# Kernel optimization log

Hardware: AMD Instinct MI355X
Metric: run time of the kernel (lower is better)

The kernel has to match this reference:

```python
import jax, jax.numpy as jnp
import numpy as np

D_MODEL = 768
D_AU = 5
D_VIS = 20
BOT = 64
WIN = 7
SCALE = 1.0 / np.sqrt(BOT).astype(np.float32)


def layernorm(x, w, b, eps=1e-5):
    mu = jnp.mean(x, axis=-1, keepdims=True)
    var = jnp.mean(jnp.square(x - mu), axis=-1, keepdims=True)
    return (x - mu) * jax.lax.rsqrt(var + eps) * w + b


def proximity_bias_matrix(prox_bias, L_a, L_v):
    # |i * (L_v/L_a) - j|, floored to int; gather into learned table, -inf outside window
    ai = jnp.arange(L_a, dtype=jnp.float32) * (L_v / L_a)  # [L_a]
    vj = jnp.arange(L_v, dtype=jnp.float32)                # [L_v]
    dist = jnp.floor(jnp.abs(ai[:, None] - vj[None, :])).astype(jnp.int32)  # [L_a, L_v]
    within = dist <= WIN
    gathered = prox_bias[jnp.clip(dist, 0, 2 * WIN)]
    return jnp.where(within, gathered, -jnp.inf)


def setup_inputs() -> dict:
    key = jax.random.key(0)
    ks = jax.random.split(key, 32)
    B, L_t, L_v, L_a = 32, 1024, 1024, 2048
    std = 0.02
    inp = {
        'x_text': jax.random.normal(ks[0], (B, L_t, D_MODEL), jnp.float32),
        'video_features': jax.random.normal(ks[1], (B, L_v, D_VIS), jnp.float32),
        'audio_features': jax.random.normal(ks[2], (B, L_a, D_AU), jnp.float32),
        # adapter input LayerNorm (BERT init: weight=1, bias=0)
        'ln_w': jnp.ones((D_MODEL,), jnp.float32),
        'ln_b': jnp.zeros((D_MODEL,), jnp.float32),
        # down projections (torch Linear: [out, in])
        'dpa_w': std * jax.random.normal(ks[3], (BOT, D_AU), jnp.float32),
        'dpa_b': jnp.zeros((BOT,), jnp.float32),
        'dpv_w': std * jax.random.normal(ks[4], (BOT, D_VIS), jnp.float32),
        'dpv_b': jnp.zeros((BOT,), jnp.float32),
        # audio->video cross attention
        'wq_a': std * jax.random.normal(ks[5], (BOT, BOT), jnp.float32),
        'wk_v': std * jax.random.normal(ks[6], (BOT, BOT), jnp.float32),
        'wv_v': std * jax.random.normal(ks[7], (BOT, BOT), jnp.float32),
        'prox_bias': jnp.zeros((2 * WIN + 1,), jnp.float32),
        # fusion MLP + LN
        'fln_w': jnp.ones((2 * BOT,), jnp.float32),
        'fln_b': jnp.zeros((2 * BOT,), jnp.float32),
        'w1f_w': std * jax.random.normal(ks[8], (BOT, 2 * BOT), jnp.float32),
        'w1f_b': jnp.zeros((BOT,), jnp.float32),
        'w2f_w': std * jax.random.normal(ks[9], (BOT, BOT), jnp.float32),
        'w2f_b': jnp.zeros((BOT,), jnp.float32),
        # text->sync alignment attention
        'wq_t': std * jax.random.normal(ks[10], (BOT, D_MODEL), jnp.float32),
        'wk_s': std * jax.random.normal(ks[11], (BOT, BOT), jnp.float32),
        'wv_s': std * jax.random.normal(ks[12], (BOT, BOT), jnp.float32),
        # up projection + learnable scalar
        'up_w': std * jax.random.normal(ks[13], (D_MODEL, BOT), jnp.float32),
        'up_b': jnp.zeros((D_MODEL,), jnp.float32),
        'scale': jnp.ones((1,), jnp.float32),
    }
    return inp


def reference(x_text, video_features, audio_features, ln_w, ln_b, dpa_w, dpa_b,
              dpv_w, dpv_b, wq_a, wk_v, wv_v, prox_bias, fln_w, fln_b,
              w1f_w, w1f_b, w2f_w, w2f_b, wq_t, wk_s, wv_s, up_w, up_b, scale):
    L_v = video_features.shape[1]
    L_a = audio_features.shape[1]
    # adapter_layernorm_option == 'in'
    xt = layernorm(x_text, ln_w, ln_b)
    # down projections + ReLU
    H_v = jax.nn.relu(jnp.einsum('bvf,df->bvd', video_features, dpv_w) + dpv_b)
    H_a = jax.nn.relu(jnp.einsum('baf,df->bad', audio_features, dpa_w) + dpa_b)
    # audio queries attend to video keys/values with proximity bias
    Q_a = jnp.einsum('bad,ed->bae', H_a, wq_a)
    K_v = jnp.einsum('bvd,ed->bve', H_v, wk_v)
    V_v = jnp.einsum('bvd,ed->bve', H_v, wv_v)
    scores = jnp.einsum('bad,bvd->bav', Q_a, K_v) * SCALE
    scores = scores + proximity_bias_matrix(prox_bias, L_a, L_v)[None]
    A = jax.nn.softmax(scores, axis=-1)  # dropout: eval-mode identity
    H_v_tilde = jnp.einsum('bav,bvd->bad', A, V_v)
    # fusion
    H_av = jnp.concatenate([H_a, H_v_tilde], axis=-1)  # [B, L_a, 2*BOT]
    H_av_n = layernorm(H_av, fln_w, fln_b)
    H_fused = jax.nn.relu(jnp.einsum('bac,dc->bad', H_av_n, w1f_w) + w1f_b)
    H_sync = jnp.einsum('bad,ed->bae', H_fused, w2f_w) + w2f_b
    # text -> sync alignment attention
    Q_t = jnp.einsum('btm,dm->btd', xt, wq_t)
    K_s = jnp.einsum('bad,ed->bae', H_sync, wk_s)
    V_s = jnp.einsum('bad,ed->bae', H_sync, wv_s)
    align = jax.nn.softmax(jnp.einsum('btd,bad->bta', Q_t, K_s) * SCALE, axis=-1)
    H_align = jnp.einsum('bta,bad->btd', align, V_s)
    up = jnp.einsum('btd,md->btm', H_align, up_w) + up_b
    return up * scale
```

## Files before the change

kernel.cpp:

```cpp
#include <hip/hip_runtime.h>

typedef unsigned short u16;
typedef unsigned int u32;

using frag8 = __attribute__((ext_vector_type(8))) short;
using facc4 = __attribute__((ext_vector_type(4))) float;

__device__ __forceinline__ float b2f(u16 u) {
  union { u32 i; float f; } v; v.i = ((u32)u) << 16; return v.f;
}
__device__ __forceinline__ u16 f2b(float f) {
  union { float f; u32 i; } v; v.f = f;
  u32 u = v.i;
  return (u16)((u + 0x7FFFu + ((u >> 16) & 1u)) >> 16);
}
__device__ __forceinline__ float ldin(const void* p, size_t i, bool bf) {
  return bf ? b2f(((const u16*)p)[i]) : ((const float*)p)[i];
}
__device__ __forceinline__ u16 ldb(const void* p, size_t i, bool bf) {
  return bf ? ((const u16*)p)[i] : f2b(((const float*)p)[i]);
}
__device__ __forceinline__ bool dt_bf16(const void* ones) {
  return *(const u32*)ones == 0x3F803F80u;
}
__device__ __forceinline__ void gload_lds16(const void* g, void* l) {
  __builtin_amdgcn_global_load_lds(
      (__attribute__((address_space(1))) void*)(g),
      (__attribute__((address_space(3))) void*)(l), 16, 0, 0);
}

#define LT 1024
#define LV 1024
#define LA 2048
#define DM 768

#define W_QA 0
#define W_KV 4096
#define W_VV 8192
#define W_1F 12288
#define W_2F 20480
#define W_KS 24576
#define W_VS 28672
#define W_UP 32768
#define W_QT 81920
#define W_TOT 131072

__global__ __launch_bounds__(256) void k_prep(
    const void* __restrict__ wqa, const void* __restrict__ wkv, const void* __restrict__ wvv,
    const void* __restrict__ w1f, const void* __restrict__ w2f,
    const void* __restrict__ wks, const void* __restrict__ wvs,
    const void* __restrict__ wup, const void* __restrict__ wqt, const void* __restrict__ lnw,
    u16* __restrict__ W)
{
  bool bf = dt_bf16(lnw);
  int idx = blockIdx.x * 256 + threadIdx.x;
  if (idx >= W_TOT) return;
  u16 v;
  if      (idx < W_KV) v = ldb(wqa, idx - W_QA, bf);
  else if (idx < W_VV) v = ldb(wkv, idx - W_KV, bf);
  else if (idx < W_1F) v = ldb(wvv, idx - W_VV, bf);
  else if (idx < W_2F) v = ldb(w1f, idx - W_1F, bf);
  else if (idx < W_KS) v = ldb(w2f, idx - W_2F, bf);
  else if (idx < W_VS) v = ldb(wks, idx - W_KS, bf);
  else if (idx < W_UP) v = ldb(wvs, idx - W_VS, bf);
  else if (idx < W_QT) v = ldb(wup, idx - W_UP, bf);
  else {
    int r = idx - W_QT;
    int k = r - (r / DM) * DM;
    v = f2b(ldin(wqt, r, bf) * ldin(lnw, k, bf));
  }
  W[idx] = v;
}

__global__ __launch_bounds__(256) void k_const(
    const u16* __restrict__ W, const void* __restrict__ wqt, const void* __restrict__ lnb,
    const void* __restrict__ dtp, float* __restrict__ CC)
{
  bool bf = dt_bf16(dtp);
  int j = blockIdx.x * 8 + (threadIdx.x >> 5);
  int lane32 = threadIdx.x & 31;
  float s = 0.f;
  if (j < 64) {
    for (int k = lane32; k < DM; k += 32) s += b2f(W[W_QT + (size_t)j * DM + k]);
  } else {
    int e = j - 64;
    for (int k = lane32; k < DM; k += 32)
      s += ldin(lnb, k, bf) * ldin(wqt, (size_t)e * DM + k, bf);
  }
#pragma unroll
  for (int m = 1; m < 32; m <<= 1) s += __shfl_xor(s, m);
  if (lane32 == 0) CC[j] = s;
}

__global__ __launch_bounds__(256) void k_video(
    const void* __restrict__ vid, const void* __restrict__ dpv_w, const void* __restrict__ dpv_b,
    const u16* __restrict__ W, const void* __restrict__ dtp,
    u16* __restrict__ KvG, u16* __restrict__ VvTG)
{
  bool bf = dt_bf16(dtp);
  __shared__ float vidT[20][72];
  __shared__ float dpvT[20][72];
  __shared__ float dpvB[64];
  __shared__ u16 hvL[64][72];
  __shared__ u16 ksS[64][72];
  __shared__ u16 vsS[64][72];
  int tid = threadIdx.x;
  int b = blockIdx.x >> 4, v0 = (blockIdx.x & 15) << 6;
  for (int c = tid; c < 1280; c += 256) {
    int row = c / 20, d = c - row * 20;
    vidT[d][row] = ldin(vid, (size_t)(b * LV + v0) * 20 + c, bf);
    dpvT[d][row] = ldin(dpv_w, c, bf);
  }
  if (tid < 64) dpvB[tid] = ldin(dpv_b, tid, bf);
  __syncthreads();
  int w = tid >> 6, ln = tid & 63;
  int quad = ln >> 4, l16 = ln & 15;
  for (int rr = 0; rr < 16; ++rr) {
    int row = w * 16 + rr;
    float h = dpvB[ln];
#pragma unroll
    for (int d = 0; d < 20; ++d) h += vidT[d][row] * dpvT[d][ln];
    hvL[row][ln] = f2b(fmaxf(h, 0.f));
  }
  facc4 ka[4] = {}, va[4] = {};
#pragma unroll
  for (int kk = 0; kk < 2; ++kk) {
    frag8 af = *(const frag8*)&hvL[w * 16 + l16][kk * 32 + quad * 8];
#pragma unroll
    for (int nt = 0; nt < 4; ++nt) {
      frag8 bk = *(const frag8*)(W + W_KV + (size_t)(nt * 16 + l16) * 64 + kk * 32 + quad * 8);
      frag8 bv = *(const frag8*)(W + W_VV + (size_t)(nt * 16 + l16) * 64 + kk * 32 + quad * 8);
      ka[nt] = __builtin_amdgcn_mfma_f32_16x16x32_bf16(af, bk, ka[nt], 0, 0, 0);
      va[nt] = __builtin_amdgcn_mfma_f32_16x16x32_bf16(af, bv, va[nt], 0, 0, 0);
    }
  }
#pragma unroll
  for (int nt = 0; nt < 4; ++nt)
#pragma unroll
    for (int r = 0; r < 4; ++r) {
      int row = w * 16 + quad * 4 + r;
      ksS[row][nt * 16 + l16] = f2b(ka[nt][r]);
      vsS[row][nt * 16 + l16] = f2b(va[nt][r]);
    }
  __syncthreads();
  for (int c = tid; c < 2048; c += 256) {
    int row = c >> 5, sg = c & 31;
    u32 v = (u32)ksS[row][sg * 2] | ((u32)ksS[row][sg * 2 + 1] << 16);
    *(u32*)(KvG + (size_t)(b * LV + v0 + row) * 64 + sg * 2) = v;
  }
  for (int c = tid; c < 2048; c += 256) {
    int e = c >> 5, sg = c & 31;
    u32 v = (u32)vsS[sg * 2][e] | ((u32)vsS[sg * 2 + 1][e] << 16);
    *(u32*)(VvTG + (size_t)(b * 64 + e) * LV + v0 + sg * 2) = v;
  }
}

__global__ __launch_bounds__(256, 2) void k_lnqt(
    const void* __restrict__ x, const u16* __restrict__ W, const float* __restrict__ CC,
    const void* __restrict__ dtp, u16* __restrict__ Qt)
{
  bool bf = dt_bf16(dtp);
  __shared__ __align__(16) char pool[65536];
  int tid = threadIdx.x;
  int w = tid >> 6, ln = tid & 63;
  int quad = ln >> 4, l16 = ln & 15;
  int R0 = blockIdx.x * 64;
  facc4 acc[4] = {};
  float s = 0.f, ss = 0.f;

  if (!bf) {
    int rqe = ln >> 4;
    const char* xb = (const char*)x + (size_t)R0 * 3072;
    const char* pe = xb + (size_t)(w * 16 + rqe) * 3072 + (((ln & 15) ^ rqe) << 4);
    const char* po = xb + (size_t)(w * 16 + 4 + rqe) * 3072 + (((ln & 15) ^ (4 + rqe)) << 4);
    const char* wgA = (const char*)(W + W_QT) +
        (size_t)(w * 16 + (ln >> 3)) * 1536 + (((ln & 7) ^ (ln >> 3)) << 4);
    const char* wgB = wgA + 8 * 1536;

#define STAGE_X(BUF, T) do { \
    size_t o_ = (size_t)(T) * 256; \
    char* lb_ = pool + (BUF) * 16384 + w * 4096; \
    gload_lds16(pe + o_,         lb_); \
    gload_lds16(po + o_,         lb_ + 1024); \
    gload_lds16(pe + 24576 + o_, lb_ + 2048); \
    gload_lds16(po + 24576 + o_, lb_ + 3072); \
  } while (0)

#define STAGE_W(BUF, T) do { \
    size_t o_ = (size_t)(T) * 128; \
    char* wb_ = pool + 49152 + (BUF) * 8192 + w * 2048; \
    gload_lds16(wgA + o_, wb_); \
    gload_lds16(wgB + o_, wb_ + 1024); \
  } while (0)

    int rbase = (w * 16 + l16) * 256;
    int r8 = l16 & 7;
    int c0a = rbase + (((quad * 2) ^ r8) << 4);
    int c0b = rbase + (((quad * 2 + 1) ^ r8) << 4);
    int c1a = rbase + (((8 + quad * 2) ^ r8) << 4);
    int c1b = rbase + (((9 + quad * 2) ^ r8) << 4);
    int wo0 = l16 * 128 + ((quad ^ r8) << 4);
    int wo1 = l16 * 128 + (((4 + quad) ^ r8) << 4);

#define COMPUTE(XB, WB) do { \
    const char* xt_ = pool + (XB) * 16384; \
    const char* wt_ = pool + 49152 + (WB) * 8192; \
    _Pragma("unroll") \
    for (int ks = 0; ks < 2; ++ks) { \
      float4 v0 = *(const float4*)(xt_ + (ks ? c1a : c0a)); \
      float4 v1 = *(const float4*)(xt_ + (ks ? c1b : c0b)); \
      s += v0.x + v0.y + v0.z + v0.w + v1.x + v1.y + v1.z + v1.w; \
      ss += v0.x * v0.x + v0.y * v0.y + v0.z * v0.z + v0.w * v0.w \
          + v1.x * v1.x + v1.y * v1.y + v1.z * v1.z + v1.w * v1.w; \
      union { u16 a[8]; frag8 f; } af; \
      af.a[0] = f2b(v0.x); af.a[1] = f2b(v0.y); af.a[2] = f2b(v0.z); af.a[3] = f2b(v0.w); \
      af.a[4] = f2b(v1.x); af.a[5] = f2b(v1.y); af.a[6] = f2b(v1.z); af.a[7] = f2b(v1.w); \
      int wo_ = ks ? wo1 : wo0; \
      _Pragma("unroll") \
      for (int nt = 0; nt < 4; ++nt) { \
        frag8 bfr = *(const frag8*)(wt_ + wo_ + nt * 2048); \
        acc[nt] = __builtin_amdgcn_mfma_f32_16x16x32_bf16(af.f, bfr, acc[nt], 0, 0, 0); \
      } \
    } \
  } while (0)

#define ITERA(T) do { \
    asm volatile("s_waitcnt vmcnt(4)" ::: "memory"); \
    __builtin_amdgcn_s_barrier(); \
    STAGE_W(((T) + 1) & 1, (T) + 1); \
    STAGE_X(((T) + 2) % 3, (T) + 2); \
    COMPUTE((T) % 3, (T) & 1); \
  } while (0)

    STAGE_W(0, 0);
    STAGE_X(0, 0);
    STAGE_X(1, 1);
    ITERA(0); ITERA(1); ITERA(2); ITERA(3); ITERA(4);
    ITERA(5); ITERA(6); ITERA(7); ITERA(8); ITERA(9);
    asm volatile("s_waitcnt vmcnt(4)" ::: "memory");
    __builtin_amdgcn_s_barrier();
    STAGE_W(1, 11);
    COMPUTE(1, 0);
    asm volatile("s_waitcnt vmcnt(0)" ::: "memory");
    __builtin_amdgcn_s_barrier();
    COMPUTE(2, 1);

#undef ITERA
#undef COMPUTE
#undef STAGE_W
#undef STAGE_X
  } else {
    const u16* xrowb = (const u16*)x + (size_t)(R0 + w * 16 + l16) * DM + quad * 8;
    for (int c = 0; c < 24; ++c) {
      union { u16 a[8]; frag8 f; } af;
      af.f = *(const frag8*)(xrowb + c * 32);
#pragma unroll
      for (int jj = 0; jj < 8; ++jj) { float v = b2f(af.a[jj]); s += v; ss += v * v; }
      int col = c * 32 + quad * 8;
#pragma unroll
      for (int nt = 0; nt < 4; ++nt) {
        frag8 bfr = *(const frag8*)(W + W_QT + (size_t)(nt * 16 + l16) * DM + col);
        acc[nt] = __builtin_amdgcn_mfma_f32_16x16x32_bf16(af.f, bfr, acc[nt], 0, 0, 0);
      }
    }
  }

  s += __shfl_xor(s, 16); ss += __shfl_xor(ss, 16);
  s += __shfl_xor(s, 32); ss += __shfl_xor(ss, 32);
  float mu = s * (1.f / 768.f);
  float var = ss * (1.f / 768.f) - mu * mu;
  float rs = rsqrtf(var + 1e-5f);
  float muR[4], rsR[4];
#pragma unroll
  for (int r = 0; r < 4; ++r) {
    muR[r] = __shfl(mu, quad * 4 + r);
    rsR[r] = __shfl(rs, quad * 4 + r);
  }
#pragma unroll
  for (int nt = 0; nt < 4; ++nt) {
    float c1 = CC[nt * 16 + l16], c2 = CC[64 + nt * 16 + l16];
#pragma unroll
    for (int r = 0; r < 4; ++r) {
      int lrow = w * 16 + quad * 4 + r;
      Qt[(size_t)(R0 + lrow) * 64 + nt * 16 + l16] =
          f2b((acc[nt][r] - muR[r] * c1) * rsR[r] * 0.125f + c2 * 0.125f);
    }
  }
}

__global__ __launch_bounds__(256) void k_audio(
    const void* __restrict__ audio, const void* __restrict__ dpa_w, const void* __restrict__ dpa_b,
    const void* __restrict__ prox_b,
    const void* __restrict__ fln_w, const void* __restrict__ fln_b,
    const void* __restrict__ w1f_b, const void* __restrict__ w2f_b,
    const u16* __restrict__ W, const void* __restrict__ dtp,
    const u16* __restrict__ KvG, const u16* __restrict__ VvTG,
    u16* __restrict__ KsG, u16* __restrict__ VsTG)
{
  bool bf = dt_bf16(dtp);
  __shared__ __align__(16) char pool[53056];
  u16* hL   = (u16*)pool;
  u16* kvB  = (u16*)(pool + 9216);
  u16* vvT  = (u16*)(pool + 16128);
  u16* qL   = (u16*)(pool + 25344);
  u16* hnL  = (u16*)(pool + 25344);
  u16* pfL  = (u16*)(pool + 42752);
  u16* hsS  = (u16*)(pool + 9216);
  u16* ksS  = (u16*)pool;
  u16* vsS  = (u16*)(pool + 9216);
  float* flnw = (float*)(pool + 51968);
  float* flnb = (float*)(pool + 52480);
  float* prox = (float*)(pool + 52992);

  int tid = threadIdx.x;
  int b = blockIdx.x >> 5, i0 = (blockIdx.x & 31) << 6;
  int w = tid >> 6, ln = tid & 63;
  int quad = ln >> 4, l16 = ln & 15;
  int jbase = (i0 >> 1) - 7;

  if (tid >= 64 && tid < 192) { int t = tid - 64; flnw[t] = ldin(fln_w, t, bf); flnb[t] = ldin(fln_b, t, bf); }
  if (tid >= 192 && tid < 207) prox[tid - 192] = ldin(prox_b, tid - 192, bf);
  for (int c = tid; c < 1536; c += 256) {
    int jr = c >> 5, ep = c & 31;
    int jj = jbase + jr; jj = jj < 0 ? 0 : (jj > LV - 1 ? LV - 1 : jj);
    *(u32*)&kvB[jr * 72 + ep * 2] = *(const u32*)(KvG + (size_t)(b * LV + jj) * 64 + ep * 2);
  }
  for (int c = tid; c < 3072; c += 256) {
    int e = c / 48, jw = c - e * 48;
    int jj = jbase + jw; jj = jj < 0 ? 0 : (jj > LV - 1 ? LV - 1 : jj);
    vvT[e * 72 + jw] = VvTG[(size_t)(b * 64 + e) * LV + jj];
  }
  for (int c = tid; c < 1024; c += 256) vvT[(c >> 4) * 72 + 48 + (c & 15)] = 0;
  __syncthreads();

  float haF[4][4];
  {
    frag8 au = {};
    if (quad == 0) {
      size_t base = (size_t)(b * LA + i0 + w * 16 + l16) * 5;
#pragma unroll
      for (int k = 0; k < 5; ++k) au[k] = (short)ldb(audio, base + k, bf);
    }
#pragma unroll
    for (int nt = 0; nt < 4; ++nt) {
      frag8 bd = {};
      if (quad == 0) {
#pragma unroll
        for (int k = 0; k < 5; ++k) bd[k] = (short)ldb(dpa_w, (size_t)(nt * 16 + l16) * 5 + k, bf);
      }
      facc4 z = {};
      facc4 ha = __builtin_amdgcn_mfma_f32_16x16x32_bf16(au, bd, z, 0, 0, 0);
      float dB = ldin(dpa_b, nt * 16 + l16, bf);
#pragma unroll
      for (int r = 0; r < 4; ++r) {
        u16 hb = f2b(fmaxf(ha[r] + dB, 0.f));
        hL[(w * 16 + quad * 4 + r) * 72 + nt * 16 + l16] = hb;
        haF[nt][r] = b2f(hb);
      }
    }
  }
  {
    facc4 qa[4] = {};
#pragma unroll
    for (int kk = 0; kk < 2; ++kk) {
      frag8 af = *(const frag8*)&hL[(w * 16 + l16) * 72 + kk * 32 + quad * 8];
#pragma unroll
      for (int nt = 0; nt < 4; ++nt) {
        frag8 bfr = *(const frag8*)(W + W_QA + (size_t)(nt * 16 + l16) * 64 + kk * 32 + quad * 8);
        qa[nt] = __builtin_amdgcn_mfma_f32_16x16x32_bf16(af, bfr, qa[nt], 0, 0, 0);
      }
    }
#pragma unroll
    for (int nt = 0; nt < 4; ++nt)
#pragma unroll
      for (int r = 0; r < 4; ++r)
        qL[(w * 16 + quad * 4 + r) * 72 + nt * 16 + l16] = f2b(qa[nt][r] * 0.125f);
  }
  float inv[4];
  {
    facc4 sa[3] = {};
#pragma unroll
    for (int kk = 0; kk < 2; ++kk) {
      frag8 af = *(const frag8*)&qL[(w * 16 + l16) * 72 + kk * 32 + quad * 8];
#pragma unroll
      for (int nt = 0; nt < 3; ++nt) {
        frag8 bfr = *(const frag8*)&kvB[(nt * 16 + l16) * 72 + kk * 32 + quad * 8];
        sa[nt] = __builtin_amdgcn_mfma_f32_16x16x32_bf16(af, bfr, sa[nt], 0, 0, 0);
      }
    }
    float den[4] = {0.f, 0.f, 0.f, 0.f};
#pragma unroll
    for (int nt = 0; nt < 3; ++nt)
#pragma unroll
      for (int r = 0; r < 4; ++r) {
        int row16 = quad * 4 + r;
        int i = i0 + w * 16 + row16;
        int j = jbase + nt * 16 + l16;
        float dist = fabsf((float)i * 0.5f - (float)j);
        float p = 0.f;
        if (j >= 0 && j < LV && dist < 8.f)
          p = exp2f(fminf(sa[nt][r] + prox[(int)dist], 60.f) * 1.44269504f);
        u16 pb = f2b(p);
        den[r] += b2f(pb);
        pfL[(w * 16 + row16) * 72 + nt * 16 + l16] = pb;
      }
#pragma unroll
    for (int r = 0; r < 4; ++r) {
      pfL[(w * 16 + quad * 4 + r) * 72 + 48 + l16] = 0;
#pragma unroll
      for (int m = 1; m < 16; m <<= 1) den[r] += __shfl_xor(den[r], m);
      inv[r] = 1.f / den[r];
    }
  }
  float hvF[4][4];
  {
    facc4 ha[4] = {};
#pragma unroll
    for (int kk = 0; kk < 2; ++kk) {
      frag8 af = *(const frag8*)&pfL[(w * 16 + l16) * 72 + kk * 32 + quad * 8];
#pragma unroll
      for (int nt = 0; nt < 4; ++nt) {
        frag8 bfr = *(const frag8*)&vvT[(nt * 16 + l16) * 72 + kk * 32 + quad * 8];
        ha[nt] = __builtin_amdgcn_mfma_f32_16x16x32_bf16(af, bfr, ha[nt], 0, 0, 0);
      }
    }
#pragma unroll
    for (int nt = 0; nt < 4; ++nt)
#pragma unroll
      for (int r = 0; r < 4; ++r) {
        u16 hb = f2b(ha[nt][r] * inv[r]);
        hvF[nt][r] = b2f(hb);
      }
  }
  __syncthreads();
#pragma unroll
  for (int r = 0; r < 4; ++r) {
    float s = 0.f, ss = 0.f;
#pragma unroll
    for (int nt = 0; nt < 4; ++nt) {
      float a = haF[nt][r], c = hvF[nt][r];
      s += a + c; ss += a * a + c * c;
    }
#pragma unroll
    for (int m = 1; m < 16; m <<= 1) { s += __shfl_xor(s, m); ss += __shfl_xor(ss, m); }
    float mu = s * (1.f / 128.f);
    float var = ss * (1.f / 128.f) - mu * mu;
    float rs = rsqrtf(var + 1e-5f);
    int row = w * 16 + quad * 4 + r;
#pragma unroll
    for (int nt = 0; nt < 4; ++nt) {
      int col = nt * 16 + l16;
      hnL[row * 136 + col]      = f2b((haF[nt][r] - mu) * rs * flnw[col] + flnb[col]);
      hnL[row * 136 + 64 + col] = f2b((hvF[nt][r] - mu) * rs * flnw[64 + col] + flnb[64 + col]);
    }
  }
  {
    facc4 f1[4] = {};
#pragma unroll
    for (int kk = 0; kk < 4; ++kk) {
      frag8 af = *(const frag8*)&hnL[(w * 16 + l16) * 136 + kk * 32 + quad * 8];
#pragma unroll
      for (int nt = 0; nt < 4; ++nt) {
        frag8 bfr = *(const frag8*)(W + W_1F + (size_t)(nt * 16 + l16) * 128 + kk * 32 + quad * 8);
        f1[nt] = __builtin_amdgcn_mfma_f32_16x16x32_bf16(af, bfr, f1[nt], 0, 0, 0);
      }
    }
#pragma unroll
    for (int nt = 0; nt < 4; ++nt) {
      float b1 = ldin(w1f_b, nt * 16 + l16, bf);
#pragma unroll
      for (int r = 0; r < 4; ++r)
        pfL[(w * 16 + quad * 4 + r) * 72 + nt * 16 + l16] = f2b(fmaxf(f1[nt][r] + b1, 0.f));
    }
  }
  {
    facc4 f2[4] = {};
#pragma unroll
    for (int kk = 0; kk < 2; ++kk) {
      frag8 af = *(const frag8*)&pfL[(w * 16 + l16) * 72 + kk * 32 + quad * 8];
#pragma unroll
      for (int nt = 0; nt < 4; ++nt) {
        frag8 bfr = *(const frag8*)(W + W_2F + (size_t)(nt * 16 + l16) * 64 + kk * 32 + quad * 8);
        f2[nt] = __builtin_amdgcn_mfma_f32_16x16x32_bf16(af, bfr, f2[nt], 0, 0, 0);
      }
    }
#pragma unroll
    for (int nt = 0; nt < 4; ++nt) {
      float b2 = ldin(w2f_b, nt * 16 + l16, bf);
#pragma unroll
      for (int r = 0; r < 4; ++r)
        hsS[(w * 16 + quad * 4 + r) * 72 + nt * 16 + l16] = f2b(f2[nt][r] + b2);
    }
  }
  {
    facc4 fk[4] = {}, fv[4] = {};
#pragma unroll
    for (int kk = 0; kk < 2; ++kk) {
      frag8 af = *(const frag8*)&hsS[(w * 16 + l16) * 72 + kk * 32 + quad * 8];
#pragma unroll
      for (int nt = 0; nt < 4; ++nt) {
        frag8 bk = *(const frag8*)(W + W_KS + (size_t)(nt * 16 + l16) * 64 + kk * 32 + quad * 8);
        frag8 bv = *(const frag8*)(W + W_VS + (size_t)(nt * 16 + l16) * 64 + kk * 32 + quad * 8);
        fk[nt] = __builtin_amdgcn_mfma_f32_16x16x32_bf16(af, bk, fk[nt], 0, 0, 0);
        fv[nt] = __builtin_amdgcn_mfma_f32_16x16x32_bf16(af, bv, fv[nt], 0, 0, 0);
      }
    }
#pragma unroll
    for (int nt = 0; nt < 4; ++nt)
#pragma unroll
      for (int r = 0; r < 4; ++r) {
        int row = w * 16 + quad * 4 + r;
        ksS[row * 72 + nt * 16 + l16] = f2b(fk[nt][r]);
        vsS[row * 72 + nt * 16 + l16] = f2b(fv[nt][r]);
      }
  }
  __syncthreads();
  for (int c = tid; c < 2048; c += 256) {
    int row = c >> 5, sg = c & 31;
    u32 v = (u32)ksS[row * 72 + sg * 2] | ((u32)ksS[row * 72 + sg * 2 + 1] << 16);
    *(u32*)(KsG + (size_t)(b * LA + i0 + row) * 64 + sg * 2) = v;
  }
  for (int c = tid; c < 2048; c += 256) {
    int e = c >> 5, sg = c & 31;
    u32 v = (u32)vsS[sg * 2 * 72 + e] | ((u32)vsS[(sg * 2 + 1) * 72 + e] << 16);
    *(u32*)(VsTG + (size_t)(b * 64 + e) * LA + i0 + sg * 2) = v;
  }
}

#define KS_OFF 0
#define VT_OFF 16384
#define PO_OFF 32768

__global__ __launch_bounds__(256, 4) void k_attn_p(
    const u16* __restrict__ Qt, const u16* __restrict__ KsG, const u16* __restrict__ VsT,
    u16* __restrict__ OpG, float* __restrict__ DenG)
{
  __shared__ __align__(16) char pool[40960];
  int tid = threadIdx.x, w = tid >> 6, ln = tid & 63;
  int quad = ln >> 4, l16 = ln & 15;
  int pb = blockIdx.x;
  int b = pb >> 5, tt = (pb >> 1) & 15, half = pb & 1;
  int t0 = tt << 6;
  const u16* qp = Qt + (size_t)(b * LT + t0 + w * 16 + l16) * 64;
  frag8 qf0 = *(const frag8*)(qp + quad * 8);
  frag8 qf1 = *(const frag8*)(qp + 32 + quad * 8);

  int r8 = ln >> 3;
  int sgx = (ln & 7) ^ r8;
  const char* kg0 = (const char*)KsG +
      (((size_t)(b * LA + half * 1024 + w * 16 + r8)) << 7) + sgx * 16;
  const char* kg1 = kg0 + 1024;
  const char* vg0 = (const char*)VsT +
      (((size_t)(b * 64 + w * 16 + r8)) * LA + half * 1024 + sgx * 8) * 2;
  const char* vg1 = vg0 + (size_t)8 * LA * 2;

#define STAGE(BUF, TT) do { \
    size_t ko_ = (size_t)(TT) * 8192, vo_ = (size_t)(TT) * 128; \
    gload_lds16(kg0 + ko_, pool + KS_OFF + (BUF) * 8192 + w * 2048); \
    gload_lds16(kg1 + ko_, pool + KS_OFF + (BUF) * 8192 + w * 2048 + 1024); \
    gload_lds16(vg0 + vo_, pool + VT_OFF + (BUF) * 8192 + w * 2048); \
    gload_lds16(vg1 + vo_, pool + VT_OFF + (BUF) * 8192 + w * 2048 + 1024); \
  } while (0)

  int l8 = l16 & 7, lh = l16 >> 3;
  int swl = l8 << 4;
  int koff0 = l16 * 128 + ((quad * 16) ^ swl);
  int koff1 = l16 * 128 + ((64 + quad * 16) ^ swl);
  int pro0 = w * 2048 + l16 * 128 + ((quad ^ l8) << 4);
  int pro1 = w * 2048 + l16 * 128 + (((4 + quad) ^ l8) << 4);
  int pwb = w * 2048 + quad * 512 + l8 * 2;

  facc4 oacc[4] = {};
  float den[4] = {0.f, 0.f, 0.f, 0.f};

#define COMPUTE(CUR) do { \
    const char* ksp_ = pool + KS_OFF + (CUR) * 8192; \
    const char* vtp_ = pool + VT_OFF + (CUR) * 8192; \
    __builtin_amdgcn_s_setprio(1); \
    _Pragma("unroll") \
    for (int nt = 0; nt < 4; ++nt) { \
      frag8 b0 = *(const frag8*)(ksp_ + koff0 + nt * 2048); \
      frag8 b1 = *(const frag8*)(ksp_ + koff1 + nt * 2048); \
      facc4 sv = {}; \
      sv = __builtin_amdgcn_mfma_f32_16x16x32_bf16(qf0, b0, sv, 0, 0, 0); \
      sv = __builtin_amdgcn_mfma_f32_16x16x32_bf16(qf1, b1, sv, 0, 0, 0); \
      _Pragma("unroll") \
      for (int r = 0; r < 4; ++r) { \
        float p = exp2f(fminf(sv[r], 60.f) * 1.44269504f); \
        u16 pb_ = f2b(p); \
        den[r] += b2f(pb_); \
        int rm_ = ((quad & 1) << 2) + r; \
        *(u16*)(pool + PO_OFF + pwb + r * 128 + (((nt * 2 + lh) ^ rm_) << 4)) = pb_; \
      } \
    } \
    _Pragma("unroll") \
    for (int kk = 0; kk < 2; ++kk) { \
      frag8 af = *(const frag8*)(pool + PO_OFF + (kk ? pro1 : pro0)); \
      _Pragma("unroll") \
      for (int nt = 0; nt < 4; ++nt) { \
        frag8 bv = *(const frag8*)(vtp_ + (kk ? koff1 : koff0) + nt * 2048); \
        oacc[nt] = __builtin_amdgcn_mfma_f32_16x16x32_bf16(af, bv, oacc[nt], 0, 0, 0); \
      } \
    } \
    __builtin_amdgcn_s_setprio(0); \
  } while (0)

#define ITERS(TT, CUR) do { \
    asm volatile("s_waitcnt vmcnt(0)" ::: "memory"); \
    __builtin_amdgcn_s_barrier(); \
    STAGE((CUR) ^ 1, (TT) + 1); \
    COMPUTE(CUR); \
  } while (0)

  STAGE(0, 0);
  for (int t2 = 0; t2 < 14; t2 += 2) {
    ITERS(t2, 0);
    ITERS(t2 + 1, 1);
  }
  ITERS(14, 0);
  asm volatile("s_waitcnt vmcnt(0)" ::: "memory");
  __builtin_amdgcn_s_barrier();
  COMPUTE(1);

#undef ITERS
#undef COMPUTE
#undef STAGE

#pragma unroll
  for (int m = 1; m < 16; m <<= 1)
#pragma unroll
    for (int r = 0; r < 4; ++r) den[r] += __shfl_xor(den[r], m);
  if (l16 == 0) {
#pragma unroll
    for (int r = 0; r < 4; ++r)
      DenG[(size_t)pb * 64 + w * 16 + quad * 4 + r] = den[r];
  }
#pragma unroll
  for (int nt = 0; nt < 4; ++nt)
#pragma unroll
    for (int r = 0; r < 4; ++r)
      OpG[(size_t)pb * 4096 + (w * 16 + quad * 4 + r) * 64 + nt * 16 + l16] =
          f2b(oacc[nt][r]);
}

__global__ __launch_bounds__(256) void k_up(
    const u16* __restrict__ OpG, const float* __restrict__ DenG,
    const u16* __restrict__ W, const void* __restrict__ up_b,
    const void* __restrict__ scaleP, const void* __restrict__ dtp, void* __restrict__ outp)
{
  bool bf = dt_bf16(dtp);
  int tid = threadIdx.x, w = tid >> 6, ln = tid & 63;
  int quad = ln >> 4, l16 = ln & 15;
  int g = blockIdx.x;
  int b = g >> 5, tt = (g >> 1) & 15, nh = g & 1;
  int t0 = tt << 6;
  int blk = b * 16 + tt;
  int row = w * 16 + l16;
  const u16* p0 = OpG + ((size_t)blk * 2 + 0) * 4096 + row * 64;
  const u16* p1 = p0 + 4096;
  float dsum = DenG[(size_t)blk * 128 + row] + DenG[(size_t)blk * 128 + 64 + row];
  float inv = 1.f / dsum;
  union { u16 a[8]; frag8 f; } a0, a1;
  {
    frag8 u0 = *(const frag8*)(p0 + quad * 8);
    frag8 u1 = *(const frag8*)(p1 + quad * 8);
    frag8 v0 = *(const frag8*)(p0 + 32 + quad * 8);
    frag8 v1 = *(const frag8*)(p1 + 32 + quad * 8);
#pragma unroll
    for (int j = 0; j < 8; ++j) {
      a0.a[j] = f2b((b2f((u16)u0[j]) + b2f((u16)u1[j])) * inv);
      a1.a[j] = f2b((b2f((u16)v0[j]) + b2f((u16)v1[j])) * inv);
    }
  }
  float scl = ldin(scaleP, 0, bf);
  u16* o16 = (u16*)outp;
  float* o32 = (float*)outp;
  for (int nt = nh * 24; nt < nh * 24 + 24; ++nt) {
    frag8 b0f = *(const frag8*)(W + W_UP + (size_t)(nt * 16 + l16) * 64 + quad * 8);
    frag8 b1f = *(const frag8*)(W + W_UP + (size_t)(nt * 16 + l16) * 64 + 32 + quad * 8);
    facc4 d = {};
    d = __builtin_amdgcn_mfma_f32_16x16x32_bf16(a0.f, b0f, d, 0, 0, 0);
    d = __builtin_amdgcn_mfma_f32_16x16x32_bf16(a1.f, b1f, d, 0, 0, 0);
    float ub = ldin(up_b, nt * 16 + l16, bf);
#pragma unroll
    for (int r = 0; r < 4; ++r) {
      int t = t0 + w * 16 + quad * 4 + r;
      size_t idx = ((size_t)(b * LT) + t) * DM + nt * 16 + l16;
      float v = (d[r] + ub) * scl;
      if (bf) o16[idx] = f2b(v); else o32[idx] = v;
    }
  }
}

extern "C" void kernel_launch(void* const* d_in, const int* in_sizes, int n_in,
                              void* d_out, int out_size, void* d_ws, size_t ws_size,
                              hipStream_t stream) {
  const void* x_text = d_in[0];
  const void* video  = d_in[1];
  const void* audio  = d_in[2];
  const void* ln_w   = d_in[3];
  const void* ln_b   = d_in[4];
  const void* dpa_w  = d_in[5];
  const void* dpa_b  = d_in[6];
  const void* dpv_w  = d_in[7];
  const void* dpv_b  = d_in[8];
  const void* wq_a   = d_in[9];
  const void* wk_v   = d_in[10];
  const void* wv_v   = d_in[11];
  const void* prox   = d_in[12];
  const void* fln_w  = d_in[13];
  const void* fln_b  = d_in[14];
  const void* w1f_w  = d_in[15];
  const void* w1f_b  = d_in[16];
  const void* w2f_w  = d_in[17];
  const void* w2f_b  = d_in[18];
  const void* wq_t   = d_in[19];
  const void* wk_s   = d_in[20];
  const void* wv_s   = d_in[21];
  const void* up_w   = d_in[22];
  const void* up_b   = d_in[23];
  const void* scale  = d_in[24];

  char* ws = (char*)d_ws;
  u16* KvG  = (u16*)(ws);
  u16* VvTG = (u16*)(ws + 4194304);
  u16* Qt   = (u16*)(ws + 8388608);
  u16* KsG  = (u16*)(ws + 12582912);
  u16* VsTG = (u16*)(ws + 20971520);
  u16* W    = (u16*)(ws + 29360128);
  float* CC = (float*)(ws + 29622272);
  u16* OpG  = (u16*)(ws);
  float* DenG = (float*)(ws + 29622784);

  k_prep <<<dim3(512), dim3(256), 0, stream>>>(wq_a, wk_v, wv_v, w1f_w, w2f_w,
                                               wk_s, wv_s, up_w, wq_t, ln_w, W);
  k_const<<<dim3(16),  dim3(256), 0, stream>>>(W, wq_t, ln_b, ln_w, CC);
  k_video<<<dim3(512), dim3(256), 0, stream>>>(video, dpv_w, dpv_b, W, ln_w, KvG, VvTG);
  k_lnqt <<<dim3(512), dim3(256), 0, stream>>>(x_text, W, CC, ln_w, Qt);
  k_audio<<<dim3(1024), dim3(256), 0, stream>>>(audio, dpa_w, dpa_b, prox,
                                                fln_w, fln_b, w1f_b, w2f_b,
                                                W, ln_w, KvG, VvTG, KsG, VsTG);
  k_attn_p<<<dim3(1024), dim3(256), 0, stream>>>(Qt, KsG, VsTG, OpG, DenG);
  k_up   <<<dim3(1024), dim3(256), 0, stream>>>(OpG, DenG, W, up_b, scale, ln_w, d_out);
}
```

Before: 376.2 us.

## Shrink LDS footprint of lnqt and audio kernels to raise occupancy

k_lnqt now handles 32 rows per block instead of 64, with two waves sharing each 16-row tile and splitting the four output column tiles. That cuts its LDS from 64KB to 40KB, doubles the grid, and raises the launch-bounds occupancy hint. k_audio aliases its separate LDS scratch buffers (h, probabilities, fused, sync, K) onto one region, shrinking LDS from about 53KB to about 37KB so more blocks fit per CU. The risk is that each x row tile is now read by two waves and each block reuses W less, and the aliasing depends on the existing barriers and per-wave row ownership being correct.

Measured after the change: 364.5 us. 1.03x faster.

```diff
diff --git a/kernel.cpp b/kernel.cpp
--- a/kernel.cpp
+++ b/kernel.cpp
@@ -155,45 +155,45 @@
   }
 }
 
-__global__ __launch_bounds__(256, 2) void k_lnqt(
+__global__ __launch_bounds__(256, 4) void k_lnqt(
     const void* __restrict__ x, const u16* __restrict__ W, const float* __restrict__ CC,
     const void* __restrict__ dtp, u16* __restrict__ Qt)
 {
   bool bf = dt_bf16(dtp);
-  __shared__ __align__(16) char pool[65536];
+  __shared__ __align__(16) char pool[40960];
   int tid = threadIdx.x;
   int w = tid >> 6, ln = tid & 63;
   int quad = ln >> 4, l16 = ln & 15;
-  int R0 = blockIdx.x * 64;
-  facc4 acc[4] = {};
+  int rt = w >> 1;
+  int nt0 = (w & 1) * 2;
+  int R0 = blockIdx.x * 32;
+  facc4 acc[2] = {};
   float s = 0.f, ss = 0.f;
 
   if (!bf) {
-    int rqe = ln >> 4;
+    int rq = ln >> 4;
     const char* xb = (const char*)x + (size_t)R0 * 3072;
-    const char* pe = xb + (size_t)(w * 16 + rqe) * 3072 + (((ln & 15) ^ rqe) << 4);
-    const char* po = xb + (size_t)(w * 16 + 4 + rqe) * 3072 + (((ln & 15) ^ (4 + rqe)) << 4);
+    const char* p0 = xb + (size_t)(w * 8 + rq) * 3072 + (((ln & 15) ^ rq) << 4);
+    const char* p1 = xb + (size_t)(w * 8 + 4 + rq) * 3072 + (((ln & 15) ^ (4 + rq)) << 4);
     const char* wgA = (const char*)(W + W_QT) +
         (size_t)(w * 16 + (ln >> 3)) * 1536 + (((ln & 7) ^ (ln >> 3)) << 4);
     const char* wgB = wgA + 8 * 1536;
 
 #define STAGE_X(BUF, T) do { \
     size_t o_ = (size_t)(T) * 256; \
-    char* lb_ = pool + (BUF) * 16384 + w * 4096; \
-    gload_lds16(pe + o_,         lb_); \
-    gload_lds16(po + o_,         lb_ + 1024); \
-    gload_lds16(pe + 24576 + o_, lb_ + 2048); \
-    gload_lds16(po + 24576 + o_, lb_ + 3072); \
+    char* lb_ = pool + (BUF) * 8192 + w * 2048; \
+    gload_lds16(p0 + o_, lb_); \
+    gload_lds16(p1 + o_, lb_ + 1024); \
   } while (0)
 
 #define STAGE_W(BUF, T) do { \
     size_t o_ = (size_t)(T) * 128; \
-    char* wb_ = pool + 49152 + (BUF) * 8192 + w * 2048; \
+    char* wb_ = pool + 24576 + (BUF) * 8192 + w * 2048; \
     gload_lds16(wgA + o_, wb_); \
     gload_lds16(wgB + o_, wb_ + 1024); \
   } while (0)
 
-    int rbase = (w * 16 + l16) * 256;
+    int rbase = (rt * 16 + l16) * 256;
     int r8 = l16 & 7;
     int c0a = rbase + (((quad * 2) ^ r8) << 4);
     int c0b = rbase + (((quad * 2 + 1) ^ r8) << 4);
@@ -203,8 +203,8 @@
     int wo1 = l16 * 128 + (((4 + quad) ^ r8) << 4);
 
 #define COMPUTE(XB, WB) do { \
-    const char* xt_ = pool + (XB) * 16384; \
-    const char* wt_ = pool + 49152 + (WB) * 8192; \
+    const char* xt_ = pool + (XB) * 8192; \
+    const char* wt_ = pool + 24576 + (WB) * 8192; \
     _Pragma("unroll") \
     for (int ks = 0; ks < 2; ++ks) { \
       float4 v0 = *(const float4*)(xt_ + (ks ? c1a : c0a)); \
@@ -217,27 +217,35 @@
       af.a[4] = f2b(v1.x); af.a[5] = f2b(v1.y); af.a[6] = f2b(v1.z); af.a[7] = f2b(v1.w); \
       int wo_ = ks ? wo1 : wo0; \
       _Pragma("unroll") \
-      for (int nt = 0; nt < 4; ++nt) { \
-        frag8 bfr = *(const frag8*)(wt_ + wo_ + nt * 2048); \
-        acc[nt] = __builtin_amdgcn_mfma_f32_16x16x32_bf16(af.f, bfr, acc[nt], 0, 0, 0); \
+      for (int n = 0; n < 2; ++n) { \
+        frag8 bfr = *(const frag8*)(wt_ + wo_ + (nt0 + n) * 2048); \
+        acc[n] = __builtin_amdgcn_mfma_f32_16x16x32_bf16(af.f, bfr, acc[n], 0, 0, 0); \
       } \
     } \
   } while (0)
 
-#define ITERA(T) do { \
-    asm volatile("s_waitcnt vmcnt(4)" ::: "memory"); \
+#define ITERA(T, XC, XN, WN) do { \
+    asm volatile("s_waitcnt vmcnt(2)" ::: "memory"); \
     __builtin_amdgcn_s_barrier(); \
-    STAGE_W(((T) + 1) & 1, (T) + 1); \
-    STAGE_X(((T) + 2) % 3, (T) + 2); \
-    COMPUTE((T) % 3, (T) & 1); \
+    STAGE_W(WN, (T) + 1); \
+    STAGE_X(XN, (T) + 2); \
+    COMPUTE(XC, (T) & 1); \
   } while (0)
 
     STAGE_W(0, 0);
     STAGE_X(0, 0);
     STAGE_X(1, 1);
-    ITERA(0); ITERA(1); ITERA(2); ITERA(3); ITERA(4);
-    ITERA(5); ITERA(6); ITERA(7); ITERA(8); ITERA(9);
-    asm volatile("s_waitcnt vmcnt(4)" ::: "memory");
+    ITERA(0, 0, 2, 1);
+    ITERA(1, 1, 0, 0);
+    ITERA(2, 2, 1, 1);
+    ITERA(3, 0, 2, 0);
+    ITERA(4, 1, 0, 1);
+    ITERA(5, 2, 1, 0);
+    ITERA(6, 0, 2, 1);
+    ITERA(7, 1, 0, 0);
+    ITERA(8, 2, 1, 1);
+    ITERA(9, 0, 2, 0);
+    asm volatile("s_waitcnt vmcnt(2)" ::: "memory");
     __builtin_amdgcn_s_barrier();
     STAGE_W(1, 11);
     COMPUTE(1, 0);
@@ -250,7 +258,7 @@
 #undef STAGE_W
 #undef STAGE_X
   } else {
-    const u16* xrowb = (const u16*)x + (size_t)(R0 + w * 16 + l16) * DM + quad * 8;
+    const u16* xrowb = (const u16*)x + (size_t)(R0 + rt * 16 + l16) * DM + quad * 8;
     for (int c = 0; c < 24; ++c) {
       union { u16 a[8]; frag8 f; } af;
       af.f = *(const frag8*)(xrowb + c * 32);
@@ -258,9 +266,9 @@
       for (int jj = 0; jj < 8; ++jj) { float v = b2f(af.a[jj]); s += v; ss += v * v; }
       int col = c * 32 + quad * 8;
 #pragma unroll
-      for (int nt = 0; nt < 4; ++nt) {
-        frag8 bfr = *(const frag8*)(W + W_QT + (size_t)(nt * 16 + l16) * DM + col);
-        acc[nt] = __builtin_amdgcn_mfma_f32_16x16x32_bf16(af.f, bfr, acc[nt], 0, 0, 0);
+      for (int n = 0; n < 2; ++n) {
+        frag8 bfr = *(const frag8*)(W + W_QT + (size_t)((nt0 + n) * 16 + l16) * DM + col);
+        acc[n] = __builtin_amdgcn_mfma_f32_16x16x32_bf16(af.f, bfr, acc[n], 0, 0, 0);
       }
     }
   }
@@ -277,18 +285,19 @@
     rsR[r] = __shfl(rs, quad * 4 + r);
   }
 #pragma unroll
-  for (int nt = 0; nt < 4; ++nt) {
-    float c1 = CC[nt * 16 + l16], c2 = CC[64 + nt * 16 + l16];
+  for (int n = 0; n < 2; ++n) {
+    int ntg = nt0 + n;
+    float c1 = CC[ntg * 16 + l16], c2 = CC[64 + ntg * 16 + l16];
 #pragma unroll
     for (int r = 0; r < 4; ++r) {
-      int lrow = w * 16 + quad * 4 + r;
-      Qt[(size_t)(R0 + lrow) * 64 + nt * 16 + l16] =
-          f2b((acc[nt][r] - muR[r] * c1) * rsR[r] * 0.125f + c2 * 0.125f);
-    }
-  }
-}
-
-__global__ __launch_bounds__(256) void k_audio(
+      int lrow = rt * 16 + quad * 4 + r;
+      Qt[(size_t)(R0 + lrow) * 64 + ntg * 16 + l16] =
+          f2b((acc[n][r] - muR[r] * c1) * rsR[r] * 0.125f + c2 * 0.125f);
+    }
+  }
+}
+
+__global__ __launch_bounds__(256, 4) void k_audio(
     const void* __restrict__ audio, const void* __restrict__ dpa_w, const void* __restrict__ dpa_b,
     const void* __restrict__ prox_b,
     const void* __restrict__ fln_w, const void* __restrict__ fln_b,
@@ -298,19 +307,16 @@
     u16* __restrict__ KsG, u16* __restrict__ VsTG)
 {
   bool bf = dt_bf16(dtp);
-  __shared__ __align__(16) char pool[53056];
-  u16* hL   = (u16*)pool;
+  __shared__ __align__(16) char pool[36928];
+  u16* S0   = (u16*)pool;
   u16* kvB  = (u16*)(pool + 9216);
   u16* vvT  = (u16*)(pool + 16128);
   u16* qL   = (u16*)(pool + 25344);
-  u16* hnL  = (u16*)(pool + 25344);
-  u16* pfL  = (u16*)(pool + 42752);
-  u16* hsS  = (u16*)(pool + 9216);
-  u16* ksS  = (u16*)pool;
+  u16* hnL  = (u16*)(pool + 18432);
   u16* vsS  = (u16*)(pool + 9216);
-  float* flnw = (float*)(pool + 51968);
-  float* flnb = (float*)(pool + 52480);
-  float* prox = (float*)(pool + 52992);
+  float* flnw = (float*)(pool + 35840);
+  float* flnb = (float*)(pool + 36352);
+  float* prox = (float*)(pool + 36864);
 
   int tid = threadIdx.x;
   int b = blockIdx.x >> 5, i0 = (blockIdx.x & 31) << 6;
@@ -354,7 +360,7 @@
 #pragma unroll
       for (int r = 0; r < 4; ++r) {
         u16 hb = f2b(fmaxf(ha[r] + dB, 0.f));
-        hL[(w * 16 + quad * 4 + r) * 72 + nt * 16 + l16] = hb;
+        S0[(w * 16 + quad * 4 + r) * 72 + nt * 16 + l16] = hb;
         haF[nt][r] = b2f(hb);
       }
     }
@@ -363,7 +369,7 @@
     facc4 qa[4] = {};
 #pragma unroll
     for (int kk = 0; kk < 2; ++kk) {
-      frag8 af = *(const frag8*)&hL[(w * 16 + l16) * 72 + kk * 32 + quad * 8];
+      frag8 af = *(const frag8*)&S0[(w * 16 + l16) * 72 + kk * 32 + quad * 8];
 #pragma unroll
       for (int nt = 0; nt < 4; ++nt) {
         frag8 bfr = *(const frag8*)(W + W_QA + (size_t)(nt * 16 + l16) * 64 + kk * 32 + quad * 8);
@@ -402,11 +408,11 @@
           p = exp2f(fminf(sa[nt][r] + prox[(int)dist], 60.f) * 1.44269504f);
         u16 pb = f2b(p);
         den[r] += b2f(pb);
-        pfL[(w * 16 + row16) * 72 + nt * 16 + l16] = pb;
+        S0[(w * 16 + row16) * 72 + nt * 16 + l16] = pb;
       }
 #pragma unroll
     for (int r = 0; r < 4; ++r) {
-      pfL[(w * 16 + quad * 4 + r) * 72 + 48 + l16] = 0;
+      S0[(w * 16 + quad * 4 + r) * 72 + 48 + l16] = 0;
 #pragma unroll
       for (int m = 1; m < 16; m <<= 1) den[r] += __shfl_xor(den[r], m);
       inv[r] = 1.f / den[r];
@@ -417,7 +423,7 @@
     facc4 ha[4] = {};
 #pragma unroll
     for (int kk = 0; kk < 2; ++kk) {
-      frag8 af = *(const frag8*)&pfL[(w * 16 + l16) * 72 + kk * 32 + quad * 8];
+      frag8 af = *(const frag8*)&S0[(w * 16 + l16) * 72 + kk * 32 + quad * 8];
 #pragma unroll
       for (int nt = 0; nt < 4; ++nt) {
         frag8 bfr = *(const frag8*)&vvT[(nt * 16 + l16) * 72 + kk * 32 + quad * 8];
@@ -470,14 +476,14 @@
       float b1 = ldin(w1f_b, nt * 16 + l16, bf);
 #pragma unroll
       for (int r = 0; r < 4; ++r)
-        pfL[(w * 16 + quad * 4 + r) * 72 + nt * 16 + l16] = f2b(fmaxf(f1[nt][r] + b1, 0.f));
+        S0[(w * 16 + quad * 4 + r) * 72 + nt * 16 + l16] = f2b(fmaxf(f1[nt][r] + b1, 0.f));
     }
   }
   {
     facc4 f2[4] = {};
 #pragma unroll
     for (int kk = 0; kk < 2; ++kk) {
-      frag8 af = *(const frag8*)&pfL[(w * 16 + l16) * 72 + kk * 32 + quad * 8];
+      frag8 af = *(const frag8*)&S0[(w * 16 + l16) * 72 + kk * 32 + quad * 8];
 #pragma unroll
       for (int nt = 0; nt < 4; ++nt) {
         frag8 bfr = *(const frag8*)(W + W_2F + (size_t)(nt * 16 + l16) * 64 + kk * 32 + quad * 8);
@@ -489,14 +495,14 @@
       float b2 = ldin(w2f_b, nt * 16 + l16, bf);
 #pragma unroll
       for (int r = 0; r < 4; ++r)
-        hsS[(w * 16 + quad * 4 + r) * 72 + nt * 16 + l16] = f2b(f2[nt][r] + b2);
+        S0[(w * 16 + quad * 4 + r) * 72 + nt * 16 + l16] = f2b(f2[nt][r] + b2);
     }
   }
   {
     facc4 fk[4] = {}, fv[4] = {};
 #pragma unroll
     for (int kk = 0; kk < 2; ++kk) {
-      frag8 af = *(const frag8*)&hsS[(w * 16 + l16) * 72 + kk * 32 + quad * 8];
+      frag8 af = *(const frag8*)&S0[(w * 16 + l16) * 72 + kk * 32 + quad * 8];
 #pragma unroll
       for (int nt = 0; nt < 4; ++nt) {
         frag8 bk = *(const frag8*)(W + W_KS + (size_t)(nt * 16 + l16) * 64 + kk * 32 + quad * 8);
@@ -510,14 +516,14 @@
 #pragma unroll
       for (int r = 0; r < 4; ++r) {
         int row = w * 16 + quad * 4 + r;
-        ksS[row * 72 + nt * 16 + l16] = f2b(fk[nt][r]);
+        S0[row * 72 + nt * 16 + l16]  = f2b(fk[nt][r]);
         vsS[row * 72 + nt * 16 + l16] = f2b(fv[nt][r]);
       }
   }
   __syncthreads();
   for (int c = tid; c < 2048; c += 256) {
     int row = c >> 5, sg = c & 31;
-    u32 v = (u32)ksS[row * 72 + sg * 2] | ((u32)ksS[row * 72 + sg * 2 + 1] << 16);
+    u32 v = (u32)S0[row * 72 + sg * 2] | ((u32)S0[row * 72 + sg * 2 + 1] << 16);
     *(u32*)(KsG + (size_t)(b * LA + i0 + row) * 64 + sg * 2) = v;
   }
   for (int c = tid; c < 2048; c += 256) {
@@ -736,7 +742,7 @@
                                                wk_s, wv_s, up_w, wq_t, ln_w, W);
   k_const<<<dim3(16),  dim3(256), 0, stream>>>(W, wq_t, ln_b, ln_w, CC);
   k_video<<<dim3(512), dim3(256), 0, stream>>>(video, dpv_w, dpv_b, W, ln_w, KvG, VvTG);
-  k_lnqt <<<dim3(512), dim3(256), 0, stream>>>(x_text, W, CC, ln_w, Qt);
+  k_lnqt <<<dim3(1024), dim3(256), 0, stream>>>(x_text, W, CC, ln_w, Qt);
   k_audio<<<dim3(1024), dim3(256), 0, stream>>>(audio, dpa_w, dpa_b, prox,
                                                 fln_w, fln_b, w1f_b, w2f_b,
                                                 W, ln_w, KvG, VvTG, KsG, VsTG);
```
